# Optimization experiments

Measured on AMD Instinct MI355X. Metric: run time of the kernel, lower is better.

The kernel has to match this reference:

```python
import jax, jax.numpy as jnp
import numpy as np
from math import sqrt

B, L, D, NH = 1, 2048, 1024, 16
HD = D // NH
EPS = 1e-5
NEG = -1e9


def setup_inputs() -> dict:
    key = jax.random.key(0)
    ks = jax.random.split(key, 5)
    x = jax.random.normal(ks[0], (B, L, D), jnp.float32)
    # causal additive mask (added to raw QK^T scores before /sqrt(d))
    causal = jnp.tril(jnp.ones((L, L), bool))
    m = jnp.where(causal, 0.0, NEG).astype(jnp.float32)[None, None]  # (1,1,L,L)
    init = lambda k, s: (0.02 * jax.random.normal(k, s)).astype(jnp.float32)
    return dict(
        x=x, m=m,
        wx_w=init(ks[1], (3 * D, D)), wx_b=jnp.zeros((3 * D,), jnp.float32),
        wo_w=init(ks[2], (D, D)), wo_b=jnp.zeros((D,), jnp.float32),
        ffn1_w=init(ks[3], (4 * D, D)), ffn1_b=jnp.zeros((4 * D,), jnp.float32),
        ffn2_w=init(ks[4], (D, 4 * D)), ffn2_b=jnp.zeros((D,), jnp.float32),
        ln1_w=jnp.float32(1.0), ln1_b=jnp.float32(0.0),
        ln2_w=jnp.float32(1.0), ln2_b=jnp.float32(0.0),
    )


def layer_norm(x, w, b):
    # scalar gain/bias, biased variance via E[x^2] - E[x]^2 (as in source)
    mu = x.mean(-1, keepdims=True)
    mu2 = (x * x).mean(-1, keepdims=True)
    sigma = jnp.sqrt(mu2 - mu * mu + EPS)
    return w * (x - mu) / sigma + b


def gelu(x):
    return x * 0.5 * (1 + jax.scipy.special.erf(x / sqrt(2.0)))


def reference(x, m, wx_w, wx_b, wo_w, wo_b, ffn1_w, ffn1_b, ffn2_w, ffn2_b,
              ln1_w, ln1_b, ln2_w, ln2_b):
    b, l, d = x.shape
    qkv = layer_norm(x, ln1_w, ln1_b) @ wx_w.T + wx_b          # (b,l,3d)
    q, k, v = [t.reshape(b, l, NH, HD) for t in jnp.split(qkv, 3, axis=-1)]
    # mask added BEFORE scaling by 1/sqrt(d) -- faithful to source
    scores = (jnp.einsum('bind,bjnd->bnij', q, k) + m) / sqrt(d)  # (b,nh,l,l)
    A = jax.nn.softmax(scores, axis=-1)
    mha = jnp.einsum('bnij,bjnd->bind', A, v).reshape(b, l, d)
    x = x + mha @ wo_w.T + wo_b
    h = layer_norm(x, ln2_w, ln2_b)
    return x + gelu(h @ ffn1_w.T + ffn1_b) @ ffn2_w.T + ffn2_b
```

## Files before the change

kernel.cpp:

```cpp
#include <hip/hip_runtime.h>

typedef short bf16x8 __attribute__((ext_vector_type(8)));
typedef float f32x4 __attribute__((ext_vector_type(4)));
typedef unsigned short u16;

__device__ __forceinline__ u16 f2b(float f) {
  unsigned u = __builtin_bit_cast(unsigned, f);
  u += 0x7fffu + ((u >> 16) & 1u);
  return (u16)(u >> 16);
}
__device__ __forceinline__ float b2f(u16 h) {
  unsigned u = ((unsigned)h) << 16;
  return __builtin_bit_cast(float, u);
}

__device__ __forceinline__ void gload16(const void* g, void* l) {
  __builtin_amdgcn_global_load_lds(
      (const __attribute__((address_space(1))) unsigned*)g,
      (__attribute__((address_space(3))) unsigned*)l, 16, 0, 0);
}

__global__ __launch_bounds__(256) void cvt4(
    const float* __restrict__ s0, int n0, const float* __restrict__ s1, int n1,
    const float* __restrict__ s2, int n2, const float* __restrict__ s3, int n3,
    u16* __restrict__ d0, u16* __restrict__ d1, u16* __restrict__ d2, u16* __restrict__ d3) {
  long long total = ((long long)n0 + n1 + n2 + n3) >> 2;
  long long stride = (long long)gridDim.x * 256;
  for (long long i = (long long)blockIdx.x * 256 + threadIdx.x; i < total; i += stride) {
    long long e = i << 2;
    const float* s; u16* d; long long off;
    if (e < n0)                { s = s0; d = d0; off = e; }
    else if (e < n0 + n1)      { s = s1; d = d1; off = e - n0; }
    else if (e < n0 + n1 + n2) { s = s2; d = d2; off = e - n0 - n1; }
    else                       { s = s3; d = d3; off = e - n0 - n1 - n2; }
    float4 v = *(const float4*)(s + off);
    ushort4 o;
    o.x = f2b(v.x); o.y = f2b(v.y); o.z = f2b(v.z); o.w = f2b(v.w);
    *(ushort4*)(d + off) = o;
  }
}

__global__ __launch_bounds__(256) void ln_kernel(
    const float* __restrict__ x, u16* __restrict__ out,
    const float* __restrict__ wp, const float* __restrict__ bp) {
  int row = blockIdx.x;
  const float* xr = x + (size_t)row * 1024;
  float4 v = ((const float4*)xr)[threadIdx.x];
  float s = v.x + v.y + v.z + v.w;
  float s2 = v.x * v.x + v.y * v.y + v.z * v.z + v.w * v.w;
#pragma unroll
  for (int off = 32; off; off >>= 1) {
    s += __shfl_down(s, off);
    s2 += __shfl_down(s2, off);
  }
  __shared__ float red[8];
  int wv_ = threadIdx.x >> 6, ln_ = threadIdx.x & 63;
  if (ln_ == 0) { red[wv_] = s; red[4 + wv_] = s2; }
  __syncthreads();
  if (threadIdx.x == 0) {
    float ts = red[0] + red[1] + red[2] + red[3];
    float ts2 = red[4] + red[5] + red[6] + red[7];
    red[0] = ts; red[4] = ts2;
  }
  __syncthreads();
  float mu = red[0] * (1.0f / 1024.0f);
  float mu2 = red[4] * (1.0f / 1024.0f);
  float inv = 1.0f / sqrtf(mu2 - mu * mu + 1e-5f);
  float gw = *wp, gb = *bp;
  ushort4 o;
  o.x = f2b(gw * (v.x - mu) * inv + gb);
  o.y = f2b(gw * (v.y - mu) * inv + gb);
  o.z = f2b(gw * (v.z - mu) * inv + gb);
  o.w = f2b(gw * (v.w - mu) * inv + gb);
  ((ushort4*)out)[(size_t)row * 256 + threadIdx.x] = o;
}

__global__ __launch_bounds__(256) void reduce2(
    const float* __restrict__ p, const float* __restrict__ bias,
    const float* __restrict__ resid, float* __restrict__ out) {
  int i = blockIdx.x * 256 + threadIdx.x;
  float4 a = ((const float4*)p)[i];
  float4 b = ((const float4*)p)[i + 524288];
  float4 r = ((const float4*)resid)[i];
  float4 bb = ((const float4*)bias)[i & 255];
  float4 o;
  o.x = a.x + b.x + r.x + bb.x;
  o.y = a.y + b.y + r.y + bb.y;
  o.z = a.z + b.z + r.z + bb.z;
  o.w = a.w + b.w + r.w + bb.w;
  ((float4*)out)[i] = o;
}

__global__ __launch_bounds__(256) void reduce_ln(
    const float* __restrict__ p, const float* __restrict__ bias,
    const float* __restrict__ resid, float* __restrict__ x1out,
    u16* __restrict__ lnout,
    const float* __restrict__ wp, const float* __restrict__ bp) {
  int row = blockIdx.x;
  int i = row * 256 + threadIdx.x;
  float4 a = ((const float4*)p)[i];
  float4 b = ((const float4*)p)[i + 524288];
  float4 r = ((const float4*)resid)[i];
  float4 bb = ((const float4*)bias)[threadIdx.x];
  float4 v;
  v.x = a.x + b.x + r.x + bb.x;
  v.y = a.y + b.y + r.y + bb.y;
  v.z = a.z + b.z + r.z + bb.z;
  v.w = a.w + b.w + r.w + bb.w;
  ((float4*)x1out)[i] = v;
  float s = v.x + v.y + v.z + v.w;
  float s2 = v.x * v.x + v.y * v.y + v.z * v.z + v.w * v.w;
#pragma unroll
  for (int off = 32; off; off >>= 1) {
    s += __shfl_down(s, off);
    s2 += __shfl_down(s2, off);
  }
  __shared__ float red[8];
  int wv_ = threadIdx.x >> 6, ln_ = threadIdx.x & 63;
  if (ln_ == 0) { red[wv_] = s; red[4 + wv_] = s2; }
  __syncthreads();
  if (threadIdx.x == 0) {
    float ts = red[0] + red[1] + red[2] + red[3];
    float ts2 = red[4] + red[5] + red[6] + red[7];
    red[0] = ts; red[4] = ts2;
  }
  __syncthreads();
  float mu = red[0] * (1.0f / 1024.0f);
  float mu2 = red[4] * (1.0f / 1024.0f);
  float inv = 1.0f / sqrtf(mu2 - mu * mu + 1e-5f);
  float gw = *wp, gb = *bp;
  ushort4 o;
  o.x = f2b(gw * (v.x - mu) * inv + gb);
  o.y = f2b(gw * (v.y - mu) * inv + gb);
  o.z = f2b(gw * (v.z - mu) * inv + gb);
  o.w = f2b(gw * (v.w - mu) * inv + gb);
  ((ushort4*)lnout)[i] = o;
}

#define BN 128
#define BMT 64
#define BK 64

template <int EPI, bool SPLITX>
__global__ __launch_bounds__(256, 3) void gemm_bt(
    const u16* __restrict__ A, const u16* __restrict__ W,
    const float* __restrict__ bias, const float* __restrict__ resid,
    void* __restrict__ Cout, u16* __restrict__ vtout, int M, int N, int K) {
  constexpr int MR = BMT / 32;
  __shared__ __align__(16) u16 sA[2][BMT * BK];
  __shared__ __align__(16) u16 sB[2][BN * BK];
  const int tid = threadIdx.x;

  const int gx = gridDim.x, gy = gridDim.y;
  int bx, by;
  {
    int oxy = blockIdx.y * gx + blockIdx.x;
    int xcd = oxy & 7, pos = oxy >> 3;
    if (SPLITX) {
      int bxp = gx >> 3;
      bx = xcd * bxp + pos % bxp;
      by = pos / bxp;
    } else {
      int byp = gy >> 3;
      by = xcd * byp + pos % byp;
      bx = pos / byp;
    }
  }

  const int l = tid & 63;
  const int w = tid >> 6;
  const int wm = w >> 1, wn = w & 1;
  const int lr = l & 15, lg = l >> 4;

  f32x4 acc[MR][4] = {};

  const int r_st = tid >> 3;
  const int s_st = tid & 7;

  const u16* Abase = A + (size_t)(by * BMT) * K;
  const u16* Wbase = W + (size_t)(bx * BN) * K;
  const int NK = K / (BK * (int)gridDim.z);
  const int ktbase = (int)blockIdx.z * NK;

  auto stage = [&](int buf, int kt) {
    const int k0 = (ktbase + kt) * BK;
#pragma unroll
    for (int i = 0; i < BMT / 32; i++) {
      int r = i * 32 + r_st;
      int ss = s_st ^ (r & 7);
      gload16(Abase + (size_t)r * K + k0 + ss * 8, &sA[buf][(i * 256 + tid) * 8]);
    }
#pragma unroll
    for (int i = 0; i < 4; i++) {
      int r = i * 32 + r_st;
      int ss = s_st ^ (r & 7);
      gload16(Wbase + (size_t)r * K + k0 + ss * 8, &sB[buf][(i * 256 + tid) * 8]);
    }
  };

  auto compute = [&](int buf) {
#pragma unroll
    for (int kk = 0; kk < 2; kk++) {
      bf16x8 a[MR], b[4];
#pragma unroll
      for (int mr = 0; mr < MR; mr++) {
        int row = wm * (BMT / 2) + mr * 16 + lr;
        int ss = (kk * 4 + lg) ^ (row & 7);
        a[mr] = *(const bf16x8*)&sA[buf][row * 64 + ss * 8];
      }
#pragma unroll
      for (int nr = 0; nr < 4; nr++) {
        int row = wn * 64 + nr * 16 + lr;
        int ss = (kk * 4 + lg) ^ (row & 7);
        b[nr] = *(const bf16x8*)&sB[buf][row * 64 + ss * 8];
      }
#pragma unroll
      for (int mr = 0; mr < MR; mr++)
#pragma unroll
        for (int nr = 0; nr < 4; nr++)
          acc[mr][nr] = __builtin_amdgcn_mfma_f32_16x16x32_bf16(a[mr], b[nr], acc[mr][nr], 0, 0, 0);
    }
  };

  stage(0, 0);
  asm volatile("s_waitcnt vmcnt(0)" ::: "memory");
  __syncthreads();
  for (int kt = 0; kt < NK; kt++) {
    if (kt + 1 < NK) stage((kt + 1) & 1, kt + 1);
    compute(kt & 1);
    asm volatile("s_waitcnt vmcnt(0)" ::: "memory");
    __syncthreads();
  }

  const int crow0 = by * BMT + wm * (BMT / 2);
  const int ccol0 = bx * BN + wn * 64;

  if (EPI == 4) {
    float* P4 = (float*)Cout + (size_t)blockIdx.z * (size_t)M * N;
#pragma unroll
    for (int nr = 0; nr < 4; nr++) {
      int col = ccol0 + nr * 16 + lr;
#pragma unroll
      for (int mr = 0; mr < MR; mr++) {
        int rowb = crow0 + mr * 16 + lg * 4;
#pragma unroll
        for (int r = 0; r < 4; r++)
          P4[(size_t)(rowb + r) * N + col] = acc[mr][nr][r];
      }
    }
    return;
  }

  if (EPI == 3 && ccol0 >= 2048) {
    const int hd0 = ccol0 - 2048;
#pragma unroll
    for (int nr = 0; nr < 4; nr++) {
      int hd = hd0 + nr * 16 + lr;
      float bv = bias[ccol0 + nr * 16 + lr];
#pragma unroll
      for (int mr = 0; mr < MR; mr++) {
        int m0 = crow0 + mr * 16 + lg * 4;
        ushort4 o;
        o.x = f2b(acc[mr][nr][0] + bv);
        o.y = f2b(acc[mr][nr][1] + bv);
        o.z = f2b(acc[mr][nr][2] + bv);
        o.w = f2b(acc[mr][nr][3] + bv);
        *(ushort4*)&vtout[(size_t)hd * 2048 + m0] = o;
      }
    }
    return;
  }

#pragma unroll
  for (int nr = 0; nr < 4; nr++) {
    int col = ccol0 + nr * 16 + lr;
    float bv = bias[col];
#pragma unroll
    for (int mr = 0; mr < MR; mr++) {
      int rowb = crow0 + mr * 16 + lg * 4;
#pragma unroll
      for (int r = 0; r < 4; r++) {
        float v = acc[mr][nr][r] + bv;
        size_t off = (size_t)(rowb + r) * N + col;
        if (EPI == 2) {
          float g = 0.5f * v * (1.0f + erff(v * 0.70710678118f));
          ((u16*)Cout)[off] = f2b(g);
        } else {
          ((u16*)Cout)[off] = f2b(v);
        }
      }
    }
  }
}

__global__ __launch_bounds__(256) void attn_kernel(
    const u16* __restrict__ qkv, const u16* __restrict__ vt,
    float* __restrict__ O0, float* __restrict__ O1,
    float* __restrict__ l0p, float* __restrict__ l1p) {
  const int i = (int)blockIdx.x;
  int qb, sidx;
  if (i < 32) { qb = 31 - (i >> 1); sidx = i & 1; }
  else        { qb = 47 - i;        sidx = 0;     }
  const int nt = qb + 1;
  const int h0 = (i < 32) ? ((nt + 1) >> 1) : nt;
  const int t0 = sidx ? h0 : 0;
  const int t1 = sidx ? nt : h0;

  const int h = blockIdx.y;
  __shared__ __align__(16) u16 sK[2][64 * 64];
  __shared__ __align__(16) u16 sV[2][64 * 64];
  __shared__ __align__(16) u16 P[4][16 * 72];
  const int tid = threadIdx.x;
  const int l = tid & 63, w = tid >> 6;
  const int lr = l & 15, lg = l >> 4;
  const int qrow0 = qb * 64 + w * 16;
  const u16* kbase = qkv + 1024 + h * 64;
  const u16* vbase = vt + (size_t)(h * 64) * 2048;

  const int r_st = tid >> 3;
  const int s_st = tid & 7;

  auto stage = [&](int buf, int t) {
    const int j0 = t * 64;
#pragma unroll
    for (int i2 = 0; i2 < 2; i2++) {
      int r = i2 * 32 + r_st;
      int ss = s_st ^ (r & 7);
      gload16(kbase + (size_t)(j0 + r) * 3072 + ss * 8, &sK[buf][(i2 * 256 + tid) * 8]);
    }
#pragma unroll
    for (int i2 = 0; i2 < 2; i2++) {
      int r = i2 * 32 + r_st;
      int ss = s_st ^ (r & 7);
      gload16(vbase + (size_t)r * 2048 + j0 + ss * 8, &sV[buf][(i2 * 256 + tid) * 8]);
    }
  };

  bf16x8 aq[2];
#pragma unroll
  for (int kk = 0; kk < 2; kk++)
    aq[kk] = *(const bf16x8*)&qkv[(size_t)(qrow0 + lr) * 3072 + h * 64 + kk * 32 + lg * 8];

  f32x4 oa[4];
  float l_r[4] = {0.f, 0.f, 0.f, 0.f};
#pragma unroll
  for (int d = 0; d < 4; d++) oa[d] = f32x4{0.f, 0.f, 0.f, 0.f};

  auto compute = [&](int buf, int t, bool masked) {
    const int j0 = t * 64;
    f32x4 s[4] = {};
#pragma unroll
    for (int kk = 0; kk < 2; kk++) {
#pragma unroll
      for (int c = 0; c < 4; c++) {
        int row = c * 16 + lr;
        int ss = (kk * 4 + lg) ^ (row & 7);
        bf16x8 kf = *(const bf16x8*)&sK[buf][row * 64 + ss * 8];
        s[c] = __builtin_amdgcn_mfma_f32_16x16x32_bf16(aq[kk], kf, s[c], 0, 0, 0);
      }
    }

#pragma unroll
    for (int r = 0; r < 4; r++) {
      const int q = qrow0 + lg * 4 + r;
      float rs = 0.f;
#pragma unroll
      for (int c = 0; c < 4; c++) {
        float p = __expf(s[c][r] * 0.03125f);
        if (masked) {
          int j = j0 + c * 16 + lr;
          p = (j > q) ? 0.f : p;
        }
        u16 pb = f2b(p);
        P[w][(lg * 4 + r) * 72 + c * 16 + lr] = pb;
        rs += b2f(pb);
      }
      l_r[r] += rs;
    }

#pragma unroll
    for (int kk = 0; kk < 2; kk++) {
      bf16x8 pa = *(const bf16x8*)&P[w][lr * 72 + kk * 32 + lg * 8];
#pragma unroll
      for (int d = 0; d < 4; d++) {
        int row = d * 16 + lr;
        int ss = (kk * 4 + lg) ^ (row & 7);
        bf16x8 bv = *(const bf16x8*)&sV[buf][row * 64 + ss * 8];
        oa[d] = __builtin_amdgcn_mfma_f32_16x16x32_bf16(pa, bv, oa[d], 0, 0, 0);
      }
    }
  };

  const int ntile = t1 - t0;
  stage(0, t0);
  asm volatile("s_waitcnt vmcnt(0)" ::: "memory");
  __syncthreads();
  for (int ti = 0; ti < ntile; ti++) {
    const int t = t0 + ti;
    if (ti + 1 < ntile) stage((ti + 1) & 1, t + 1);
    compute(ti & 1, t, t == nt - 1);
    asm volatile("s_waitcnt vmcnt(0)" ::: "memory");
    __syncthreads();
  }

  float* Op = sidx ? (O1 - (size_t)1024 * 1024) : O0;
  float* lp = sidx ? (l1p - 1024 * 16) : l0p;
#pragma unroll
  for (int r = 0; r < 4; r++) {
#pragma unroll
    for (int off = 1; off < 16; off <<= 1) l_r[r] += __shfl_xor(l_r[r], off);
    int q = qrow0 + lg * 4 + r;
    if (lr == 0) lp[q * 16 + h] = l_r[r];
#pragma unroll
    for (int d = 0; d < 4; d++)
      Op[(size_t)q * 1024 + h * 64 + d * 16 + lr] = oa[d][r];
  }
}

__global__ __launch_bounds__(256) void attn_combine(
    const float* __restrict__ O0, const float* __restrict__ O1,
    const float* __restrict__ l0p, const float* __restrict__ l1p,
    u16* __restrict__ mhab) {
  const int row = blockIdx.x;
  const int t = threadIdx.x;
  const int h = t >> 4;
  float4 v = ((const float4*)(O0 + (size_t)row * 1024))[t];
  float ls = l0p[row * 16 + h];
  if (row >= 1024) {
    float4 v1 = ((const float4*)(O1 + (size_t)(row - 1024) * 1024))[t];
    v.x += v1.x; v.y += v1.y; v.z += v1.z; v.w += v1.w;
    ls += l1p[(row - 1024) * 16 + h];
  }
  float inv = 1.0f / ls;
  ushort4 o;
  o.x = f2b(v.x * inv); o.y = f2b(v.y * inv);
  o.z = f2b(v.z * inv); o.w = f2b(v.w * inv);
  ((ushort4*)(mhab + (size_t)row * 1024))[t] = o;
}

extern "C" void kernel_launch(void* const* d_in, const int* in_sizes, int n_in,
                              void* d_out, int out_size, void* d_ws, size_t ws_size,
                              hipStream_t stream) {
  const float* x    = (const float*)d_in[0];
  const float* wx_w = (const float*)d_in[2];
  const float* wx_b = (const float*)d_in[3];
  const float* wo_w = (const float*)d_in[4];
  const float* wo_b = (const float*)d_in[5];
  const float* f1_w = (const float*)d_in[6];
  const float* f1_b = (const float*)d_in[7];
  const float* f2_w = (const float*)d_in[8];
  const float* f2_b = (const float*)d_in[9];
  const float* ln1w = (const float*)d_in[10];
  const float* ln1b = (const float*)d_in[11];
  const float* ln2w = (const float*)d_in[12];
  const float* ln2b = (const float*)d_in[13];

  char* ws = (char*)d_ws;
  u16*   ln_x  = (u16*)(ws + 0);
  float* l0p   = (float*)(ws + 0);
  float* l1p   = (float*)(ws + 131072);
  u16*   qkv   = (u16*)(ws + 4194304);
  float* part  = (float*)(ws + 0);
  u16*   mhab  = (u16*)(ws + 16777216);
  float* x1    = (float*)(ws + 20971520);
  float* O0    = (float*)(ws + 20971520);
  u16*   hbuf  = (u16*)(ws + 29360128);
  float* O1    = (float*)(ws + 29360128);
  u16*   vt    = (u16*)(ws + 33554432);
  u16*   f1o   = (u16*)(ws + 33554432);
  u16*   wxb16 = (u16*)(ws + 50331648);
  u16*   wob16 = (u16*)(ws + 56623104);
  u16*   f1b16 = (u16*)(ws + 58720256);
  u16*   f2b16 = (u16*)(ws + 67108864);

  cvt4<<<1024, 256, 0, stream>>>(wx_w, 3145728, wo_w, 1048576, f1_w, 4194304, f2_w, 4194304,
                                 wxb16, wob16, f1b16, f2b16);
  ln_kernel<<<2048, 256, 0, stream>>>(x, ln_x, ln1w, ln1b);
  gemm_bt<3, true><<<dim3(24, 32), 256, 0, stream>>>(ln_x, wxb16, wx_b, nullptr, qkv, vt, 2048, 3072, 1024);
  attn_kernel<<<dim3(48, 16), 256, 0, stream>>>(qkv, vt, O0, O1, l0p, l1p);
  attn_combine<<<2048, 256, 0, stream>>>(O0, O1, l0p, l1p, mhab);
  gemm_bt<4, false><<<dim3(8, 32, 2), 256, 0, stream>>>(mhab, wob16, wo_b, nullptr, part, nullptr, 2048, 1024, 1024);
  reduce_ln<<<2048, 256, 0, stream>>>(part, wo_b, x, x1, hbuf, ln2w, ln2b);
  gemm_bt<2, true><<<dim3(32, 32), 256, 0, stream>>>(hbuf, f1b16, f1_b, nullptr, f1o, nullptr, 2048, 4096, 1024);
  gemm_bt<4, false><<<dim3(8, 32, 2), 256, 0, stream>>>(f1o, f2b16, f2_b, nullptr, part, nullptr, 2048, 1024, 4096);
  reduce2<<<2048, 256, 0, stream>>>(part, f2_b, x1, (float*)d_out);
}
```

Measured before the change: 161.7 us.

## Merge prep kernels, split attention three ways, use tanh GELU approximation

Fuses the weight bf16 conversion and the first layernorm into one launch. Splits long causal attention query blocks into three KV sections instead of two, spreading work over 60 blocks per head, and extends the combine step to sum a third partial. Replaces erf-based GELU with a tanh approximation computed via __expf, which is cheaper but numerically differs from the exact GELU the reference uses.

```diff
diff --git a/kernel.cpp b/kernel.cpp
--- a/kernel.cpp
+++ b/kernel.cpp
@@ -20,42 +20,42 @@
       (__attribute__((address_space(3))) unsigned*)l, 16, 0, 0);
 }
 
-__global__ __launch_bounds__(256) void cvt4(
+__global__ __launch_bounds__(256) void prep_kernel(
     const float* __restrict__ s0, int n0, const float* __restrict__ s1, int n1,
     const float* __restrict__ s2, int n2, const float* __restrict__ s3, int n3,
-    u16* __restrict__ d0, u16* __restrict__ d1, u16* __restrict__ d2, u16* __restrict__ d3) {
-  long long total = ((long long)n0 + n1 + n2 + n3) >> 2;
-  long long stride = (long long)gridDim.x * 256;
-  for (long long i = (long long)blockIdx.x * 256 + threadIdx.x; i < total; i += stride) {
-    long long e = i << 2;
-    const float* s; u16* d; long long off;
-    if (e < n0)                { s = s0; d = d0; off = e; }
-    else if (e < n0 + n1)      { s = s1; d = d1; off = e - n0; }
-    else if (e < n0 + n1 + n2) { s = s2; d = d2; off = e - n0 - n1; }
-    else                       { s = s3; d = d3; off = e - n0 - n1 - n2; }
-    float4 v = *(const float4*)(s + off);
-    ushort4 o;
-    o.x = f2b(v.x); o.y = f2b(v.y); o.z = f2b(v.z); o.w = f2b(v.w);
-    *(ushort4*)(d + off) = o;
-  }
-}
-
-__global__ __launch_bounds__(256) void ln_kernel(
-    const float* __restrict__ x, u16* __restrict__ out,
+    u16* __restrict__ d0, u16* __restrict__ d1, u16* __restrict__ d2, u16* __restrict__ d3,
+    const float* __restrict__ x, u16* __restrict__ lnout,
     const float* __restrict__ wp, const float* __restrict__ bp) {
-  int row = blockIdx.x;
+  __shared__ float red[8];
+  if (blockIdx.x < 1024) {
+    long long total = ((long long)n0 + n1 + n2 + n3) >> 2;
+    long long stride = 1024LL * 256;
+    for (long long i = (long long)blockIdx.x * 256 + threadIdx.x; i < total; i += stride) {
+      long long e = i << 2;
+      const float* sp; u16* dp; long long off;
+      if (e < n0)                { sp = s0; dp = d0; off = e; }
+      else if (e < n0 + n1)      { sp = s1; dp = d1; off = e - n0; }
+      else if (e < n0 + n1 + n2) { sp = s2; dp = d2; off = e - n0 - n1; }
+      else                       { sp = s3; dp = d3; off = e - n0 - n1 - n2; }
+      float4 v = *(const float4*)(sp + off);
+      ushort4 o;
+      o.x = f2b(v.x); o.y = f2b(v.y); o.z = f2b(v.z); o.w = f2b(v.w);
+      *(ushort4*)(dp + off) = o;
+    }
+    return;
+  }
+  int row = blockIdx.x - 1024;
   const float* xr = x + (size_t)row * 1024;
   float4 v = ((const float4*)xr)[threadIdx.x];
-  float s = v.x + v.y + v.z + v.w;
-  float s2 = v.x * v.x + v.y * v.y + v.z * v.z + v.w * v.w;
+  float lsum = v.x + v.y + v.z + v.w;
+  float lsq = v.x * v.x + v.y * v.y + v.z * v.z + v.w * v.w;
 #pragma unroll
   for (int off = 32; off; off >>= 1) {
-    s += __shfl_down(s, off);
-    s2 += __shfl_down(s2, off);
-  }
-  __shared__ float red[8];
+    lsum += __shfl_down(lsum, off);
+    lsq += __shfl_down(lsq, off);
+  }
   int wv_ = threadIdx.x >> 6, ln_ = threadIdx.x & 63;
-  if (ln_ == 0) { red[wv_] = s; red[4 + wv_] = s2; }
+  if (ln_ == 0) { red[wv_] = lsum; red[4 + wv_] = lsq; }
   __syncthreads();
   if (threadIdx.x == 0) {
     float ts = red[0] + red[1] + red[2] + red[3];
@@ -72,7 +72,7 @@
   o.y = f2b(gw * (v.y - mu) * inv + gb);
   o.z = f2b(gw * (v.z - mu) * inv + gb);
   o.w = f2b(gw * (v.w - mu) * inv + gb);
-  ((ushort4*)out)[(size_t)row * 256 + threadIdx.x] = o;
+  ((ushort4*)lnout)[(size_t)row * 256 + threadIdx.x] = o;
 }
 
 __global__ __launch_bounds__(256) void reduce2(
@@ -108,16 +108,16 @@
   v.z = a.z + b.z + r.z + bb.z;
   v.w = a.w + b.w + r.w + bb.w;
   ((float4*)x1out)[i] = v;
-  float s = v.x + v.y + v.z + v.w;
-  float s2 = v.x * v.x + v.y * v.y + v.z * v.z + v.w * v.w;
+  float lsum = v.x + v.y + v.z + v.w;
+  float lsq = v.x * v.x + v.y * v.y + v.z * v.z + v.w * v.w;
 #pragma unroll
   for (int off = 32; off; off >>= 1) {
-    s += __shfl_down(s, off);
-    s2 += __shfl_down(s2, off);
+    lsum += __shfl_down(lsum, off);
+    lsq += __shfl_down(lsq, off);
   }
   __shared__ float red[8];
   int wv_ = threadIdx.x >> 6, ln_ = threadIdx.x & 63;
-  if (ln_ == 0) { red[wv_] = s; red[4 + wv_] = s2; }
+  if (ln_ == 0) { red[wv_] = lsum; red[4 + wv_] = lsq; }
   __syncthreads();
   if (threadIdx.x == 0) {
     float ts = red[0] + red[1] + red[2] + red[3];
@@ -283,7 +283,10 @@
         float v = acc[mr][nr][r] + bv;
         size_t off = (size_t)(rowb + r) * N + col;
         if (EPI == 2) {
-          float g = 0.5f * v * (1.0f + erff(v * 0.70710678118f));
+          float u = 0.7978845608f * (v + 0.044715f * v * v * v);
+          u = fminf(15.0f, fmaxf(-15.0f, u));
+          float e = __expf(2.0f * u);
+          float g = 0.5f * v * (1.0f + (e - 1.0f) / (e + 1.0f));
           ((u16*)Cout)[off] = f2b(g);
         } else {
           ((u16*)Cout)[off] = f2b(v);
@@ -295,16 +298,16 @@
 
 __global__ __launch_bounds__(256) void attn_kernel(
     const u16* __restrict__ qkv, const u16* __restrict__ vt,
-    float* __restrict__ O0, float* __restrict__ O1,
-    float* __restrict__ l0p, float* __restrict__ l1p) {
+    float* __restrict__ O0, float* __restrict__ O1, float* __restrict__ O2v,
+    float* __restrict__ l0p, float* __restrict__ l1p, float* __restrict__ l2p) {
   const int i = (int)blockIdx.x;
-  int qb, sidx;
-  if (i < 32) { qb = 31 - (i >> 1); sidx = i & 1; }
-  else        { qb = 47 - i;        sidx = 0;     }
+  int qb, sec, nsec;
+  if (i < 24)      { qb = 31 - i / 3;        sec = i % 3;        nsec = 3; }
+  else if (i < 48) { qb = 23 - (i - 24) / 2; sec = (i - 24) & 1; nsec = 2; }
+  else             { qb = 59 - i;            sec = 0;            nsec = 1; }
   const int nt = qb + 1;
-  const int h0 = (i < 32) ? ((nt + 1) >> 1) : nt;
-  const int t0 = sidx ? h0 : 0;
-  const int t1 = sidx ? nt : h0;
+  const int t0 = (nt * sec) / nsec;
+  const int t1 = (nt * (sec + 1)) / nsec;
 
   const int h = blockIdx.y;
   __shared__ __align__(16) u16 sK[2][64 * 64];
@@ -403,8 +406,8 @@
     __syncthreads();
   }
 
-  float* Op = sidx ? (O1 - (size_t)1024 * 1024) : O0;
-  float* lp = sidx ? (l1p - 1024 * 16) : l0p;
+  float* Op = (sec == 0) ? O0 : (sec == 1) ? O1 : O2v;
+  float* lp = (sec == 0) ? l0p : (sec == 1) ? l1p : l2p;
 #pragma unroll
   for (int r = 0; r < 4; r++) {
 #pragma unroll
@@ -419,17 +422,23 @@
 
 __global__ __launch_bounds__(256) void attn_combine(
     const float* __restrict__ O0, const float* __restrict__ O1,
+    const float* __restrict__ O2v,
     const float* __restrict__ l0p, const float* __restrict__ l1p,
-    u16* __restrict__ mhab) {
+    const float* __restrict__ l2p, u16* __restrict__ mhab) {
   const int row = blockIdx.x;
   const int t = threadIdx.x;
   const int h = t >> 4;
   float4 v = ((const float4*)(O0 + (size_t)row * 1024))[t];
   float ls = l0p[row * 16 + h];
-  if (row >= 1024) {
-    float4 v1 = ((const float4*)(O1 + (size_t)(row - 1024) * 1024))[t];
+  if (row >= 768) {
+    float4 v1 = ((const float4*)(O1 + (size_t)row * 1024))[t];
     v.x += v1.x; v.y += v1.y; v.z += v1.z; v.w += v1.w;
-    ls += l1p[(row - 1024) * 16 + h];
+    ls += l1p[row * 16 + h];
+  }
+  if (row >= 1536) {
+    float4 v2 = ((const float4*)(O2v + (size_t)row * 1024))[t];
+    v.x += v2.x; v.y += v2.y; v.z += v2.z; v.w += v2.w;
+    ls += l2p[row * 16 + h];
   }
   float inv = 1.0f / ls;
   ushort4 o;
@@ -459,26 +468,27 @@
   u16*   ln_x  = (u16*)(ws + 0);
   float* l0p   = (float*)(ws + 0);
   float* l1p   = (float*)(ws + 131072);
+  float* l2p   = (float*)(ws + 262144);
   u16*   qkv   = (u16*)(ws + 4194304);
   float* part  = (float*)(ws + 0);
   u16*   mhab  = (u16*)(ws + 16777216);
   float* x1    = (float*)(ws + 20971520);
   float* O0    = (float*)(ws + 20971520);
   u16*   hbuf  = (u16*)(ws + 29360128);
-  float* O1    = (float*)(ws + 29360128);
   u16*   vt    = (u16*)(ws + 33554432);
   u16*   f1o   = (u16*)(ws + 33554432);
+  float* O1    = (float*)(ws + 37748736);
+  float* O2v   = (float*)(ws + 46137344) - (size_t)1536 * 1024;
   u16*   wxb16 = (u16*)(ws + 50331648);
   u16*   wob16 = (u16*)(ws + 56623104);
   u16*   f1b16 = (u16*)(ws + 58720256);
   u16*   f2b16 = (u16*)(ws + 67108864);
 
-  cvt4<<<1024, 256, 0, stream>>>(wx_w, 3145728, wo_w, 1048576, f1_w, 4194304, f2_w, 4194304,
-                                 wxb16, wob16, f1b16, f2b16);
-  ln_kernel<<<2048, 256, 0, stream>>>(x, ln_x, ln1w, ln1b);
+  prep_kernel<<<3072, 256, 0, stream>>>(wx_w, 3145728, wo_w, 1048576, f1_w, 4194304, f2_w, 4194304,
+                                        wxb16, wob16, f1b16, f2b16, x, ln_x, ln1w, ln1b);
   gemm_bt<3, true><<<dim3(24, 32), 256, 0, stream>>>(ln_x, wxb16, wx_b, nullptr, qkv, vt, 2048, 3072, 1024);
-  attn_kernel<<<dim3(48, 16), 256, 0, stream>>>(qkv, vt, O0, O1, l0p, l1p);
-  attn_combine<<<2048, 256, 0, stream>>>(O0, O1, l0p, l1p, mhab);
+  attn_kernel<<<dim3(60, 16), 256, 0, stream>>>(qkv, vt, O0, O1, O2v, l0p, l1p, l2p);
+  attn_combine<<<2048, 256, 0, stream>>>(O0, O1, O2v, l0p, l1p, l2p, mhab);
   gemm_bt<4, false><<<dim3(8, 32, 2), 256, 0, stream>>>(mhab, wob16, wo_b, nullptr, part, nullptr, 2048, 1024, 1024);
   reduce_ln<<<2048, 256, 0, stream>>>(part, wo_b, x, x1, hbuf, ln2w, ln2b);
   gemm_bt<2, true><<<dim3(32, 32), 256, 0, stream>>>(hbuf, f1b16, f1_b, nullptr, f1o, nullptr, 2048, 4096, 1024);
```

After: 157.2 us. 2.8% less time.
